# Kernel tuning notes

Hardware: AMD Instinct MI355X
Metric: run time of the kernel (lower is better)

## Reference

```python
import jax, jax.numpy as jnp
import numpy as np

B, L = 64, 16384
INTERP_FACTOR = 0.25
WINDOW, STEP = 256, 64
ALPHA, BETA, TEMP = 0.12, 0.9, 1.0
A = -0.75  # PyTorch grid_sample bicubic coefficient


def _cubic_w(t):
    # cubic convolution kernel (Keys, a=-0.75), matches torch bicubic
    at = jnp.abs(t)
    w_near = ((A + 2.0) * at - (A + 3.0)) * at * at + 1.0          # |t| <= 1
    w_far = ((A * at - 5.0 * A) * at + 8.0 * A) * at - 4.0 * A      # 1 < |t| < 2
    return jnp.where(at <= 1.0, w_near, jnp.where(at < 2.0, w_far, 0.0))


def cubic_interpolate_1d(signal, interp_factor):
    # equivalent to the grid_sample(mode='bicubic', padding='border',
    # align_corners=True) hack on a (B,1,1,n) image: y-direction is identity.
    b, n = signal.shape
    num_points = int((n - 1) / interp_factor) + 1
    x = jnp.linspace(0.0, 1.0, num_points) * (n - 1)                 # sample coords
    i0 = jnp.floor(x).astype(jnp.int32)
    frac = x - i0.astype(x.dtype)
    offs = jnp.arange(-1, 3)                                         # 4 taps
    idx = jnp.clip(i0[:, None] + offs[None, :], 0, n - 1)            # (P,4) border pad
    w = _cubic_w(frac[:, None] - offs[None, :].astype(x.dtype))      # (P,4)
    taps = signal[:, idx]                                            # (B,P,4)
    return jnp.einsum('bpk,pk->bp', taps, w)


def _apply_kernels(x):
    # gamma-normalized mix: 0.5*polynomial(deg=2,off=1.3) + 0.5*gaussian(c=0.7,s=1.0)
    poly = (x + 1.3) ** 2
    gauss = jnp.exp(-0.5 * ((x - 0.7) / 1.0) ** 2)
    return 0.5 * poly + 0.5 * gauss


def soft_minimum(a, b, temperature):
    b = jnp.broadcast_to(b, a.shape)
    stacked = jnp.stack([-a * temperature, -b * temperature], axis=0)
    return -jax.nn.logsumexp(stacked, axis=0) / temperature


def _forward(signal):
    interp = cubic_interpolate_1d(signal, INTERP_FACTOR)             # (B, n)
    n = interp.shape[1]
    n_windows = (n - WINDOW) // STEP + 1
    starts = jnp.arange(n_windows) * STEP
    idx = starts[:, None] + jnp.arange(WINDOW)[None, :]              # (nw, W)
    windows = interp[:, idx]                                         # (B, nw, W)
    kw = _apply_kernels(windows)                                     # per-window kernel eval
    M = jnp.abs(jnp.fft.fft(kw, axis=-1))                            # magnitude spectrum
    Mmax = jnp.max(M, axis=-1, keepdims=True)
    thr = ALPHA * Mmax                                               # local threshold
    mask = jax.nn.sigmoid((M - thr) * TEMP)                          # soft threshold
    Mt = M * mask
    return soft_minimum(Mt, BETA * Mmax, TEMP)                       # smart min (B, nw, W)


def setup_inputs() -> dict:
    key = jax.random.key(0)
    return {"signal": jax.random.normal(key, (B, L), dtype=jnp.float32)}


def reference(signal):
    return _forward(signal)
```

## Files before the change

kernel.cpp:

```cpp
#include <hip/hip_runtime.h>
#include <math.h>

#define LSIG 16384
#define NWIN 1020
#define WTILE 64
#define MTILES 16
#define STRIP 1088
#define RBSTRIDE 260
#define RBOFF (STRIP * 8)
#define PMAXOFF (RBOFF + 16 * RBSTRIDE * 4)
#define LDSBYTES (PMAXOFF + 32 * 4 * 4)

typedef __attribute__((ext_vector_type(8))) short short8;
typedef __attribute__((ext_vector_type(4))) float f32x4;
typedef __attribute__((ext_vector_type(4))) unsigned short us4;

__device__ __forceinline__ unsigned short f2b(float f) {
    union { float f; unsigned int u; } x; x.f = f;
    unsigned int r = x.u + 0x7fffu + ((x.u >> 16) & 1u);
    return (unsigned short)(r >> 16);
}

__device__ __forceinline__ float kwf(float x) {
    float p = x + 1.3f;
    float d = x - 0.7f;
    return fmaf(0.5f * p, p, 0.5f * __expf(-0.5f * d * d));
}

__device__ __forceinline__ float smin_fast(float Mv, float thr, float bb) {
    float t = __expf(thr - Mv);
    float Mt = Mv * __builtin_amdgcn_rcpf(1.0f + t);
    return fminf(Mt, bb);
}

__global__ void build_dft(unsigned short* __restrict__ Bf) {
    const int t = blockIdx.x;
    const int c = threadIdx.x;
    const int bin = ((c >> 6) << 5) + (((c >> 5) & 1) << 4) + (c & 15);
    const int kind = (c >> 4) & 1;
    float v;
    if (c == 16) {
        v = (t & 1) ? -1.0f : 1.0f;
    } else {
        const int prod = (bin * t) & 255;
        const float a = (float)prod * 0.024543692606170f;
        v = (kind == 0) ? __cosf(a) : -__sinf(a);
    }
    Bf[(((t >> 3) * 256) + c) * 8 + (t & 7)] = f2b(v);
}

__global__ __launch_bounds__(256, 4) void ntfa_gemm(const float* __restrict__ sig,
                                                    const unsigned short* __restrict__ Bf,
                                                    float* __restrict__ out) {
    __shared__ __align__(16) char lds[LDSBYTES];
    float* rb = (float*)(lds + RBOFF);
    float* pmax_s = (float*)(lds + PMAXOFF);

    const int tid = threadIdx.x;
    const int lane = tid & 63;
    const int wid = tid >> 6;
    const int wn0 = wid * 64;
    const int lm = lane & 15;
    const int lg = lane >> 4;
    const bool spec = (wid == 0) && (lm == 0);

    const int mtile = blockIdx.x;
    const int b = blockIdx.y;
    const int S0q = mtile * 1024;
    const float* srow = sig + (size_t)b * LSIG;

#pragma unroll
    for (int k = 0; k < 5; ++k) {
        int q = tid + k * 256;
        if (q < STRIP) {
            int gq = S0q + q;
            float o0 = 0.f, o1 = 0.f, o2 = 0.f, o3 = 0.f;
            if (gq <= 16383) {
                float ta = srow[gq - 1 < 0 ? 0 : gq - 1];
                float tb = srow[gq];
                float tc = srow[gq + 1 > 16383 ? 16383 : gq + 1];
                float td = srow[gq + 2 > 16383 ? 16383 : gq + 2];
                float x0 = tb;
                float x1 = fmaf(ta, -0.10546875f, fmaf(tb, 0.87890625f,
                            fmaf(tc, 0.26171875f, td * -0.03515625f)));
                float x2 = fmaf(ta, -0.09375f, fmaf(tb, 0.59375f,
                            fmaf(tc, 0.59375f, td * -0.09375f)));
                float x3 = fmaf(ta, -0.03515625f, fmaf(tb, 0.26171875f,
                            fmaf(tc, 0.87890625f, td * -0.10546875f)));
                o0 = kwf(x0); o1 = kwf(x1); o2 = kwf(x2); o3 = kwf(x3);
                if (gq == 16383) { o1 = 0.f; o2 = 0.f; o3 = 0.f; }
            }
            us4 pk; pk.x = f2b(o0); pk.y = f2b(o1); pk.z = f2b(o2); pk.w = f2b(o3);
            int la = q * 8;
            la ^= ((la >> 7) & 7) << 4;
            *(us4*)(lds + la) = pk;
        }
    }
    __syncthreads();

    const int w0 = mtile * WTILE;

#pragma unroll
    for (int ph = 0; ph < 2; ++ph) {
        f32x4 acc[2][4] = {};
        short8 bcur[4], bnxt[4];
#pragma unroll
        for (int nt = 0; nt < 4; ++nt)
            bcur[nt] = *(const short8*)(Bf + ((0 * 4 + lg) * 256 + wn0 + nt * 16 + lm) * 8);
#pragma unroll
        for (int ks = 0; ks < 8; ++ks) {
            if (ks < 7) {
#pragma unroll
                for (int nt = 0; nt < 4; ++nt)
                    bnxt[nt] = *(const short8*)(Bf + (((ks + 1) * 4 + lg) * 256 + wn0 + nt * 16 + lm) * 8);
            }
            short8 afr[2];
#pragma unroll
            for (int mt = 0; mt < 2; ++mt) {
                int sb = ((ph * 32 + mt * 16 + lm) * 64 + ks * 32 + lg * 8) * 2;
                sb ^= ((sb >> 7) & 7) << 4;
                afr[mt] = *(const short8*)(lds + sb);
            }
#pragma unroll
            for (int mt = 0; mt < 2; ++mt)
#pragma unroll
                for (int nt = 0; nt < 4; ++nt)
                    acc[mt][nt] = __builtin_amdgcn_mfma_f32_16x16x32_bf16(
                        afr[mt], bcur[nt], acc[mt][nt], 0, 0, 0);
            if (ks < 7) {
#pragma unroll
                for (int nt = 0; nt < 4; ++nt) bcur[nt] = bnxt[nt];
            }
        }

        float M[2][2][4], M128[2][4], pm[2][4];
#pragma unroll
        for (int mt = 0; mt < 2; ++mt) {
#pragma unroll
            for (int k = 0; k < 2; ++k)
#pragma unroll
                for (int r = 0; r < 4; ++r) {
                    float re = acc[mt][2 * k][r];
                    float im = acc[mt][2 * k + 1][r];
                    if (k == 0 && spec) {
                        M[mt][0][r] = fabsf(re);
                        M128[mt][r] = fabsf(im);
                    } else {
                        M[mt][k][r] = __builtin_amdgcn_sqrtf(fmaf(re, re, im * im));
                    }
                }
#pragma unroll
            for (int r = 0; r < 4; ++r) {
                float p = fmaxf(M[mt][0][r], M[mt][1][r]);
                if (spec) p = fmaxf(p, M128[mt][r]);
                pm[mt][r] = p;
            }
        }
#pragma unroll
        for (int msk = 1; msk < 16; msk <<= 1)
#pragma unroll
            for (int mt = 0; mt < 2; ++mt)
#pragma unroll
                for (int r = 0; r < 4; ++r)
                    pm[mt][r] = fmaxf(pm[mt][r], __shfl_xor(pm[mt][r], msk));

        if (lm == 0) {
#pragma unroll
            for (int mt = 0; mt < 2; ++mt)
#pragma unroll
                for (int r = 0; r < 4; ++r)
                    pmax_s[(mt * 16 + lg * 4 + r) * 4 + wid] = pm[mt][r];
        }
        __syncthreads();

#pragma unroll
        for (int mt = 0; mt < 2; ++mt) {
#pragma unroll
            for (int r = 0; r < 4; ++r) {
                const int win16 = lg * 4 + r;
                const float* pp = pmax_s + (mt * 16 + win16) * 4;
                const float Mx = fmaxf(fmaxf(pp[0], pp[1]), fmaxf(pp[2], pp[3]));
                const float thr = 0.12f * Mx;
                const float bb = 0.9f * Mx;
                float* row = rb + win16 * RBSTRIDE;
#pragma unroll
                for (int k = 0; k < 2; ++k) {
                    const int bin = wid * 32 + k * 16 + lm;
                    const float outv = smin_fast(M[mt][k][r], thr, bb);
                    row[bin] = outv;
                    row[256 - bin] = outv;
                    if (k == 0 && spec)
                        row[128] = smin_fast(M128[mt][r], thr, bb);
                }
            }
            __syncthreads();
            {
                const int r16 = lane >> 4;
                const int f4c = lane & 15;
                const int win16s = wid * 4 + r16;
                const int gw = w0 + ph * 32 + mt * 16 + win16s;
                if (gw < NWIN) {
                    const float* rrow = rb + win16s * RBSTRIDE;
                    float* orow = out + (((size_t)(b * NWIN + gw)) << 8);
#pragma unroll
                    for (int it = 0; it < 4; ++it) {
                        const int c4 = f4c + it * 16;
                        f32x4 v = *(const f32x4*)(rrow + c4 * 4);
                        __builtin_nontemporal_store(v, (f32x4*)(orow + c4 * 4));
                    }
                }
            }
            __syncthreads();
        }
    }
}

extern "C" void kernel_launch(void* const* d_in, const int* in_sizes, int n_in,
                              void* d_out, int out_size, void* d_ws, size_t ws_size,
                              hipStream_t stream) {
    const float* sig = (const float*)d_in[0];
    float* out = (float*)d_out;
    unsigned short* Bf = (unsigned short*)d_ws;

    hipLaunchKernelGGL(build_dft, dim3(256), dim3(256), 0, stream, Bf);
    hipLaunchKernelGGL(ntfa_gemm, dim3(MTILES, 64), dim3(256), 0, stream, sig, Bf, out);
}
```

Before: 30.50 us.

## Halve windows per block to double grid size and drop B-fragment prefetch

Each block now handles 32 windows instead of 64, so the grid doubles to 32x64 blocks and the strip staged in LDS shrinks to 576 entries. The two-phase loop goes away, and the register double-buffered prefetch of DFT B fragments is replaced by direct per-k-step loads paired with MFMAs. Launch bounds are raised to 8 blocks per CU to allow higher occupancy. In exchange, B fragments are reloaded per block twice as often across the grid, the strip overlap becomes a larger share of each block's interpolation work, and the loss of explicit prefetch may expose global load latency.

```diff
diff --git a/kernel.cpp b/kernel.cpp
--- a/kernel.cpp
+++ b/kernel.cpp
@@ -3,9 +3,9 @@
 
 #define LSIG 16384
 #define NWIN 1020
-#define WTILE 64
-#define MTILES 16
-#define STRIP 1088
+#define WTILE 32
+#define MTILES 32
+#define STRIP 576
 #define RBSTRIDE 260
 #define RBOFF (STRIP * 8)
 #define PMAXOFF (RBOFF + 16 * RBSTRIDE * 4)
@@ -49,7 +49,7 @@
     Bf[(((t >> 3) * 256) + c) * 8 + (t & 7)] = f2b(v);
 }
 
-__global__ __launch_bounds__(256, 4) void ntfa_gemm(const float* __restrict__ sig,
+__global__ __launch_bounds__(256, 8) void ntfa_gemm(const float* __restrict__ sig,
                                                     const unsigned short* __restrict__ Bf,
                                                     float* __restrict__ out) {
     __shared__ __align__(16) char lds[LDSBYTES];
@@ -66,11 +66,11 @@
 
     const int mtile = blockIdx.x;
     const int b = blockIdx.y;
-    const int S0q = mtile * 1024;
+    const int S0q = mtile * 512;
     const float* srow = sig + (size_t)b * LSIG;
 
 #pragma unroll
-    for (int k = 0; k < 5; ++k) {
+    for (int k = 0; k < 3; ++k) {
         int q = tid + k * 256;
         if (q < STRIP) {
             int gq = S0q + q;
@@ -98,120 +98,106 @@
     }
     __syncthreads();
 
+    f32x4 acc[2][4] = {};
+#pragma unroll
+    for (int ks = 0; ks < 8; ++ks) {
+        short8 afr[2];
+#pragma unroll
+        for (int mt = 0; mt < 2; ++mt) {
+            int sb = ((mt * 16 + lm) * 64 + ks * 32 + lg * 8) * 2;
+            sb ^= ((sb >> 7) & 7) << 4;
+            afr[mt] = *(const short8*)(lds + sb);
+        }
+#pragma unroll
+        for (int np = 0; np < 2; ++np) {
+            short8 bp0 = *(const short8*)(Bf + ((ks * 4 + lg) * 256 + wn0 + (2 * np) * 16 + lm) * 8);
+            short8 bp1 = *(const short8*)(Bf + ((ks * 4 + lg) * 256 + wn0 + (2 * np + 1) * 16 + lm) * 8);
+            acc[0][2 * np]     = __builtin_amdgcn_mfma_f32_16x16x32_bf16(afr[0], bp0, acc[0][2 * np], 0, 0, 0);
+            acc[0][2 * np + 1] = __builtin_amdgcn_mfma_f32_16x16x32_bf16(afr[0], bp1, acc[0][2 * np + 1], 0, 0, 0);
+            acc[1][2 * np]     = __builtin_amdgcn_mfma_f32_16x16x32_bf16(afr[1], bp0, acc[1][2 * np], 0, 0, 0);
+            acc[1][2 * np + 1] = __builtin_amdgcn_mfma_f32_16x16x32_bf16(afr[1], bp1, acc[1][2 * np + 1], 0, 0, 0);
+        }
+    }
+
+    float M[2][2][4], M128[2][4], pm[2][4];
+#pragma unroll
+    for (int mt = 0; mt < 2; ++mt) {
+#pragma unroll
+        for (int k = 0; k < 2; ++k)
+#pragma unroll
+            for (int r = 0; r < 4; ++r) {
+                float re = acc[mt][2 * k][r];
+                float im = acc[mt][2 * k + 1][r];
+                if (k == 0 && spec) {
+                    M[mt][0][r] = fabsf(re);
+                    M128[mt][r] = fabsf(im);
+                } else {
+                    M[mt][k][r] = __builtin_amdgcn_sqrtf(fmaf(re, re, im * im));
+                }
+            }
+#pragma unroll
+        for (int r = 0; r < 4; ++r) {
+            float p = fmaxf(M[mt][0][r], M[mt][1][r]);
+            if (spec) p = fmaxf(p, M128[mt][r]);
+            pm[mt][r] = p;
+        }
+    }
+#pragma unroll
+    for (int msk = 1; msk < 16; msk <<= 1)
+#pragma unroll
+        for (int mt = 0; mt < 2; ++mt)
+#pragma unroll
+            for (int r = 0; r < 4; ++r)
+                pm[mt][r] = fmaxf(pm[mt][r], __shfl_xor(pm[mt][r], msk));
+
+    if (lm == 0) {
+#pragma unroll
+        for (int mt = 0; mt < 2; ++mt)
+#pragma unroll
+            for (int r = 0; r < 4; ++r)
+                pmax_s[(mt * 16 + lg * 4 + r) * 4 + wid] = pm[mt][r];
+    }
+    __syncthreads();
+
     const int w0 = mtile * WTILE;
-
-#pragma unroll
-    for (int ph = 0; ph < 2; ++ph) {
-        f32x4 acc[2][4] = {};
-        short8 bcur[4], bnxt[4];
-#pragma unroll
-        for (int nt = 0; nt < 4; ++nt)
-            bcur[nt] = *(const short8*)(Bf + ((0 * 4 + lg) * 256 + wn0 + nt * 16 + lm) * 8);
-#pragma unroll
-        for (int ks = 0; ks < 8; ++ks) {
-            if (ks < 7) {
-#pragma unroll
-                for (int nt = 0; nt < 4; ++nt)
-                    bnxt[nt] = *(const short8*)(Bf + (((ks + 1) * 4 + lg) * 256 + wn0 + nt * 16 + lm) * 8);
-            }
-            short8 afr[2];
-#pragma unroll
-            for (int mt = 0; mt < 2; ++mt) {
-                int sb = ((ph * 32 + mt * 16 + lm) * 64 + ks * 32 + lg * 8) * 2;
-                sb ^= ((sb >> 7) & 7) << 4;
-                afr[mt] = *(const short8*)(lds + sb);
-            }
-#pragma unroll
-            for (int mt = 0; mt < 2; ++mt)
-#pragma unroll
-                for (int nt = 0; nt < 4; ++nt)
-                    acc[mt][nt] = __builtin_amdgcn_mfma_f32_16x16x32_bf16(
-                        afr[mt], bcur[nt], acc[mt][nt], 0, 0, 0);
-            if (ks < 7) {
-#pragma unroll
-                for (int nt = 0; nt < 4; ++nt) bcur[nt] = bnxt[nt];
-            }
-        }
-
-        float M[2][2][4], M128[2][4], pm[2][4];
-#pragma unroll
-        for (int mt = 0; mt < 2; ++mt) {
-#pragma unroll
-            for (int k = 0; k < 2; ++k)
-#pragma unroll
-                for (int r = 0; r < 4; ++r) {
-                    float re = acc[mt][2 * k][r];
-                    float im = acc[mt][2 * k + 1][r];
-                    if (k == 0 && spec) {
-                        M[mt][0][r] = fabsf(re);
-                        M128[mt][r] = fabsf(im);
-                    } else {
-                        M[mt][k][r] = __builtin_amdgcn_sqrtf(fmaf(re, re, im * im));
-                    }
+#pragma unroll
+    for (int mt = 0; mt < 2; ++mt) {
+#pragma unroll
+        for (int r = 0; r < 4; ++r) {
+            const int win16 = lg * 4 + r;
+            const float* pp = pmax_s + (mt * 16 + win16) * 4;
+            const float Mx = fmaxf(fmaxf(pp[0], pp[1]), fmaxf(pp[2], pp[3]));
+            const float thr = 0.12f * Mx;
+            const float bb = 0.9f * Mx;
+            float* row = rb + win16 * RBSTRIDE;
+#pragma unroll
+            for (int k = 0; k < 2; ++k) {
+                const int bin = wid * 32 + k * 16 + lm;
+                const float outv = smin_fast(M[mt][k][r], thr, bb);
+                row[bin] = outv;
+                row[256 - bin] = outv;
+                if (k == 0 && spec)
+                    row[128] = smin_fast(M128[mt][r], thr, bb);
+            }
+        }
+        __syncthreads();
+        {
+            const int r16 = lane >> 4;
+            const int f4c = lane & 15;
+            const int win16s = wid * 4 + r16;
+            const int gw = w0 + mt * 16 + win16s;
+            if (gw < NWIN) {
+                const float* rrow = rb + win16s * RBSTRIDE;
+                float* orow = out + (((size_t)(b * NWIN + gw)) << 8);
+#pragma unroll
+                for (int it = 0; it < 4; ++it) {
+                    const int c4 = f4c + it * 16;
+                    f32x4 v = *(const f32x4*)(rrow + c4 * 4);
+                    __builtin_nontemporal_store(v, (f32x4*)(orow + c4 * 4));
                 }
-#pragma unroll
-            for (int r = 0; r < 4; ++r) {
-                float p = fmaxf(M[mt][0][r], M[mt][1][r]);
-                if (spec) p = fmaxf(p, M128[mt][r]);
-                pm[mt][r] = p;
-            }
-        }
-#pragma unroll
-        for (int msk = 1; msk < 16; msk <<= 1)
-#pragma unroll
-            for (int mt = 0; mt < 2; ++mt)
-#pragma unroll
-                for (int r = 0; r < 4; ++r)
-                    pm[mt][r] = fmaxf(pm[mt][r], __shfl_xor(pm[mt][r], msk));
-
-        if (lm == 0) {
-#pragma unroll
-            for (int mt = 0; mt < 2; ++mt)
-#pragma unroll
-                for (int r = 0; r < 4; ++r)
-                    pmax_s[(mt * 16 + lg * 4 + r) * 4 + wid] = pm[mt][r];
+            }
         }
         __syncthreads();
-
-#pragma unroll
-        for (int mt = 0; mt < 2; ++mt) {
-#pragma unroll
-            for (int r = 0; r < 4; ++r) {
-                const int win16 = lg * 4 + r;
-                const float* pp = pmax_s + (mt * 16 + win16) * 4;
-                const float Mx = fmaxf(fmaxf(pp[0], pp[1]), fmaxf(pp[2], pp[3]));
-                const float thr = 0.12f * Mx;
-                const float bb = 0.9f * Mx;
-                float* row = rb + win16 * RBSTRIDE;
-#pragma unroll
-                for (int k = 0; k < 2; ++k) {
-                    const int bin = wid * 32 + k * 16 + lm;
-                    const float outv = smin_fast(M[mt][k][r], thr, bb);
-                    row[bin] = outv;
-                    row[256 - bin] = outv;
-                    if (k == 0 && spec)
-                        row[128] = smin_fast(M128[mt][r], thr, bb);
-                }
-            }
-            __syncthreads();
-            {
-                const int r16 = lane >> 4;
-                const int f4c = lane & 15;
-                const int win16s = wid * 4 + r16;
-                const int gw = w0 + ph * 32 + mt * 16 + win16s;
-                if (gw < NWIN) {
-                    const float* rrow = rb + win16s * RBSTRIDE;
-                    float* orow = out + (((size_t)(b * NWIN + gw)) << 8);
-#pragma unroll
-                    for (int it = 0; it < 4; ++it) {
-                        const int c4 = f4c + it * 16;
-                        f32x4 v = *(const f32x4*)(rrow + c4 * 4);
-                        __builtin_nontemporal_store(v, (f32x4*)(orow + c4 * 4));
-                    }
-                }
-            }
-            __syncthreads();
-        }
     }
 }
 
```

Measured after the change: 30.22 us, median of 2. No clear change (-0.9%).
